# Kernel optimization log

Measured on AMD Instinct MI355X. Metric: run time of the kernel, lower is better.

The kernel has to match this reference:

```python
import jax, jax.numpy as jnp
import numpy as np
import math

D_MODEL = 1024
N_HEADS = 16
HEAD_DIM = D_MODEL // N_HEADS
SEQ_LEN = 8192
INCLUDE_LOCAL = 2


def get_dilated_positions(seq_len, include_local=2):
    # Faithful numpy port of the torch pattern generator (runs once at setup).
    max_attend = include_local + int(math.ceil(math.log2(seq_len + 1)))
    positions = np.zeros((seq_len, max_attend), dtype=np.int64)
    mask = np.zeros((seq_len, max_attend), dtype=bool)
    for i in range(seq_len):
        ap = [i]
        for j in range(1, include_local + 1):
            if i - j >= 0:
                ap.append(i - j)
        k = 2
        while i - 2 ** k >= 0:
            ap.append(i - 2 ** k)
            k += 1
        positions[i, :len(ap)] = ap
        mask[i, :len(ap)] = True
    return positions, mask


def setup_inputs() -> dict:
    key = jax.random.key(0)
    kx, kq, kk, kv, ko = jax.random.split(key, 5)
    x = jax.random.normal(kx, (1, SEQ_LEN, D_MODEL), dtype=jnp.float32)
    # nn.Linear(bias=False) weights, torch layout [out_features, in_features]
    s = 0.02
    q_w = jax.random.normal(kq, (D_MODEL, D_MODEL), dtype=jnp.float32) * s
    k_w = jax.random.normal(kk, (D_MODEL, D_MODEL), dtype=jnp.float32) * s
    v_w = jax.random.normal(kv, (D_MODEL, D_MODEL), dtype=jnp.float32) * s
    o_w = jax.random.normal(ko, (D_MODEL, D_MODEL), dtype=jnp.float32) * s
    pos_np, mask_np = get_dilated_positions(SEQ_LEN, INCLUDE_LOCAL)
    return {
        "x": x,
        "q_w": q_w, "k_w": k_w, "v_w": v_w, "o_w": o_w,
        "positions": jnp.asarray(pos_np),   # (S, A) int64 indices
        "attend_mask": jnp.asarray(mask_np) # (S, A) bool
    }


def reference(x, q_w, k_w, v_w, o_w, positions, attend_mask):
    B, S, _ = x.shape
    H, Dh = N_HEADS, HEAD_DIM
    scale = Dh ** -0.5

    q = (x @ q_w.T).reshape(B, S, H, Dh).transpose(0, 2, 1, 3)  # (B,H,S,Dh)
    k = (x @ k_w.T).reshape(B, S, H, Dh).transpose(0, 2, 1, 3)
    v = (x @ v_w.T).reshape(B, S, H, Dh).transpose(0, 2, 1, 3)

    # Gather K/V at the dilated positions: (B,H,S,A,Dh)
    k_sparse = k[:, :, positions, :]
    v_sparse = v[:, :, positions, :]

    scores = jnp.einsum('bhsd,bhsad->bhsa', q, k_sparse) * scale
    scores = jnp.where(attend_mask[None, None, :, :], scores, -jnp.inf)
    attn = jax.nn.softmax(scores, axis=-1)  # dropout p in eval / 0.0 -> identity

    out = jnp.einsum('bhsa,bhsad->bhsd', attn, v_sparse)
    out = out.transpose(0, 2, 1, 3).reshape(B, S, D_MODEL)
    return out @ o_w.T
```

## Files before the change

### kernel.cpp

```cpp
#include <hip/hip_runtime.h>
#include <hip/hip_bf16.h>

typedef __bf16 bf16_t;
typedef __bf16 bf16x4 __attribute__((ext_vector_type(4)));
typedef __bf16 bf16x8 __attribute__((ext_vector_type(8)));
typedef float floatx16 __attribute__((ext_vector_type(16)));

#define SEQ    8192
#define DM     1024
#define NHEADS 16
#define HDIM   64

__device__ __forceinline__ void async_ld16(bf16_t* lds, const bf16_t* g) {
  __builtin_amdgcn_global_load_lds(
      (__attribute__((address_space(1))) void*)g,
      (__attribute__((address_space(3))) void*)lds, 16, 0, 0);
}

__global__ __launch_bounds__(256)
void cvt_all(const float* __restrict__ x,  const float* __restrict__ qw,
             const float* __restrict__ kw, const float* __restrict__ vw,
             const float* __restrict__ ow,
             bf16_t* __restrict__ Xb,  bf16_t* __restrict__ QWb,
             bf16_t* __restrict__ KWb, bf16_t* __restrict__ VWb,
             bf16_t* __restrict__ OWb) {
  const int b = blockIdx.x;
  const float* in; bf16_t* out; int g;
  if (b < 8192) { in = x; out = Xb; g = b; }
  else {
    const int w  = (b - 8192) >> 10;
    const int wb = (b - 8192) & 1023;
    switch (w) {
      case 0:  in = qw; out = QWb; break;
      case 1:  in = kw; out = KWb; break;
      case 2:  in = vw; out = VWb; break;
      default: in = ow; out = OWb; break;
    }
    g = wb;
  }
  const int idx = (g * 256 + threadIdx.x) * 4;
  float4 v = *(const float4*)(in + idx);
  bf16x4 o = { (bf16_t)v.x, (bf16_t)v.y, (bf16_t)v.z, (bf16_t)v.w };
  *(bf16x4*)(out + idx) = o;
}

template <typename OutT>
__device__ __forceinline__ void gemm_core_256x128(
    const bf16_t* __restrict__ A, const bf16_t* __restrict__ B,
    OutT* __restrict__ C, float scl)
{
  constexpr int Kdim = DM;
  constexpr int NT   = Kdim / 64;
  __shared__ __attribute__((aligned(16))) bf16_t sA[2][256 * 64];
  __shared__ __attribute__((aligned(16))) bf16_t sB[2][128 * 64];

  const int tid  = threadIdx.x;
  const int wave = tid >> 6;
  const int lane = tid & 63;
  const int l31  = lane & 31;
  const int half = lane >> 5;
  const int wm   = wave >> 1;
  const int wn   = wave & 1;

  const int gc = (lane & 7) ^ ((lane >> 3) & 7);
  const size_t arow = (size_t)blockIdx.x * 256 + wave * 8 + (lane >> 3);
  const size_t brow = (size_t)blockIdx.y * 128 + wave * 8 + (lane >> 3);
  const bf16_t* Ag = A + arow * Kdim + gc * 8;
  const bf16_t* Bg = B + brow * Kdim + gc * 8;

  floatx16 acc[2][2];
  #pragma unroll
  for (int i = 0; i < 2; ++i)
    #pragma unroll
    for (int j = 0; j < 2; ++j)
      acc[i][j] = (floatx16)(0.0f);

  #pragma unroll
  for (int j = 0; j < 4; ++j)
    async_ld16(&sA[0][(j * 64 + wave * 8) * 64], Ag + (size_t)j * 64 * Kdim);
  #pragma unroll
  for (int j = 0; j < 2; ++j)
    async_ld16(&sB[0][(j * 64 + wave * 8) * 64], Bg + (size_t)j * 64 * Kdim);
  __syncthreads();

  const int sw = l31 & 7;

  for (int kt = 0; kt < NT; ++kt) {
    const int  cur = kt & 1;
    const int  nxt = cur ^ 1;
    const int  ko  = (kt + 1) * 64;
    const bool pre = (kt + 1 < NT);

    #pragma unroll
    for (int s = 0; s < 4; ++s) {
      const int slot = ((s * 2 + half) ^ sw) * 8;
      bf16x8 af0 = *(const bf16x8*)&sA[cur][(wm * 64      + l31) * 64 + slot];
      bf16x8 af1 = *(const bf16x8*)&sA[cur][(wm * 64 + 32 + l31) * 64 + slot];
      bf16x8 bf0 = *(const bf16x8*)&sB[cur][(wn * 64      + l31) * 64 + slot];
      bf16x8 bf1 = *(const bf16x8*)&sB[cur][(wn * 64 + 32 + l31) * 64 + slot];

      if (pre) {
        if (s == 0) {
          async_ld16(&sA[nxt][(0 * 64 + wave * 8) * 64], Ag + (size_t)0 * 64 * Kdim + ko);
          async_ld16(&sA[nxt][(1 * 64 + wave * 8) * 64], Ag + (size_t)1 * 64 * Kdim + ko);
        } else if (s == 1) {
          async_ld16(&sA[nxt][(2 * 64 + wave * 8) * 64], Ag + (size_t)2 * 64 * Kdim + ko);
          async_ld16(&sA[nxt][(3 * 64 + wave * 8) * 64], Ag + (size_t)3 * 64 * Kdim + ko);
        } else if (s == 2) {
          async_ld16(&sB[nxt][(0 * 64 + wave * 8) * 64], Bg + ko);
          async_ld16(&sB[nxt][(1 * 64 + wave * 8) * 64], Bg + (size_t)64 * Kdim + ko);
        }
      }

      __builtin_amdgcn_s_barrier();
      __builtin_amdgcn_s_setprio(1);
      acc[0][0] = __builtin_amdgcn_mfma_f32_32x32x16_bf16(af0, bf0, acc[0][0], 0, 0, 0);
      acc[0][1] = __builtin_amdgcn_mfma_f32_32x32x16_bf16(af0, bf1, acc[0][1], 0, 0, 0);
      acc[1][0] = __builtin_amdgcn_mfma_f32_32x32x16_bf16(af1, bf0, acc[1][0], 0, 0, 0);
      acc[1][1] = __builtin_amdgcn_mfma_f32_32x32x16_bf16(af1, bf1, acc[1][1], 0, 0, 0);
      __builtin_amdgcn_s_setprio(0);
      if (s < 3) __builtin_amdgcn_s_barrier();
    }

    __syncthreads();
  }

  const int crow0 = blockIdx.x * 256 + wm * 64 + 4 * half;
  const int ccol0 = blockIdx.y * 128 + wn * 64 + l31;
  #pragma unroll
  for (int mi = 0; mi < 2; ++mi)
    #pragma unroll
    for (int ni = 0; ni < 2; ++ni)
      #pragma unroll
      for (int r = 0; r < 16; ++r) {
        const int row = crow0 + mi * 32 + (r & 3) + 8 * (r >> 2);
        C[(size_t)row * DM + (ccol0 + ni * 32)] = (OutT)(acc[mi][ni][r] * scl);
      }
}

__global__ __launch_bounds__(512, 2)
void gemm_qkv(const bf16_t* __restrict__ A,
              const bf16_t* __restrict__ Bq, const bf16_t* __restrict__ Bk,
              const bf16_t* __restrict__ Bv,
              bf16_t* __restrict__ Cq, bf16_t* __restrict__ Ck, bf16_t* __restrict__ Cv)
{
  const bf16_t* B = (blockIdx.z == 0) ? Bq : (blockIdx.z == 1) ? Bk : Bv;
  bf16_t*       C = (blockIdx.z == 0) ? Cq : (blockIdx.z == 1) ? Ck : Cv;
  const float scl = (blockIdx.z == 0) ? 0.125f : 1.0f;
  gemm_core_256x128<bf16_t>(A, B, C, scl);
}

__global__ __launch_bounds__(512, 2)
void gemm_out(const bf16_t* __restrict__ A, const bf16_t* __restrict__ B,
              float* __restrict__ C)
{
  gemm_core_256x128<float>(A, B, C, 1.0f);
}

__global__ __launch_bounds__(256)
void dilated_attn(const bf16_t* __restrict__ Q, const bf16_t* __restrict__ K,
                  const bf16_t* __restrict__ V, bf16_t* O)
{
  __shared__ float sM[2][64];
  __shared__ float sL[2][64];
  __shared__ float sAcc[2][64][17];

  const int lane = threadIdx.x & 63;
  const int wv   = threadIdx.x >> 6;
  const int ql   = wv >> 1;
  const int sub  = wv & 1;
  const int qb   = (blockIdx.x & 7) * 512 + (blockIdx.x >> 3);
  const int i    = qb * 2 + ql;
  const size_t base = (size_t)i * DM + lane * 16;

  bf16x8 q0 = *(const bf16x8*)(Q + base);
  bf16x8 q1 = *(const bf16x8*)(Q + base + 8);
  float qf[16];
  #pragma unroll
  for (int j = 0; j < 8; ++j) { qf[j] = (float)q0[j]; qf[j + 8] = (float)q1[j]; }

  const int npos = (i == 0) ? 1 : (33 - __builtin_clz((unsigned)i));
  auto pos_addr = [&](int t) -> size_t {
    const int off = (t == 0) ? 0 : (1 << (t - 1));
    return (size_t)(i - off) * DM + lane * 16;
  };

  float m = -INFINITY, l = 0.0f;
  float acc[16];
  #pragma unroll
  for (int j = 0; j < 16; ++j) acc[j] = 0.0f;

  int t = sub;
  if (t < npos) {
    size_t a = pos_addr(t);
    bf16x8 k0 = *(const bf16x8*)(K + a), k1 = *(const bf16x8*)(K + a + 8);
    bf16x8 v0 = *(const bf16x8*)(V + a), v1 = *(const bf16x8*)(V + a + 8);
    while (true) {
      const int tn = t + 2;
      const bool more = (tn < npos);
      bf16x8 nk0, nk1, nv0, nv1;
      if (more) {
        const size_t na = pos_addr(tn);
        nk0 = *(const bf16x8*)(K + na); nk1 = *(const bf16x8*)(K + na + 8);
        nv0 = *(const bf16x8*)(V + na); nv1 = *(const bf16x8*)(V + na + 8);
      }

      float sc = 0.0f;
      #pragma unroll
      for (int j = 0; j < 8; ++j) sc += qf[j] * (float)k0[j] + qf[j + 8] * (float)k1[j];
      sc += __shfl_xor(sc, 1, 64);
      sc += __shfl_xor(sc, 2, 64);

      float mn = fmaxf(m, sc);
      float co = __expf(m - mn);
      float w  = __expf(sc - mn);
      l = l * co + w;
      m = mn;
      #pragma unroll
      for (int j = 0; j < 8; ++j) {
        acc[j]     = acc[j]     * co + w * (float)v0[j];
        acc[j + 8] = acc[j + 8] * co + w * (float)v1[j];
      }

      if (!more) break;
      k0 = nk0; k1 = nk1; v0 = nv0; v1 = nv1;
      t = tn;
    }
  }

  if (sub == 1) {
    sM[ql][lane] = m;
    sL[ql][lane] = l;
    #pragma unroll
    for (int j = 0; j < 16; ++j) sAcc[ql][lane][j] = acc[j];
  }
  __syncthreads();
  if (sub == 0) {
    const float mb = sM[ql][lane], lb = sL[ql][lane];
    const float mt = fmaxf(m, mb);
    const float ca = __expf(m - mt);
    const float cb = __expf(mb - mt);
    const float inv = 1.0f / (l * ca + lb * cb);
    bf16x8 o0, o1;
    #pragma unroll
    for (int j = 0; j < 8; ++j) {
      o0[j] = (bf16_t)((acc[j]     * ca + sAcc[ql][lane][j]     * cb) * inv);
      o1[j] = (bf16_t)((acc[j + 8] * ca + sAcc[ql][lane][j + 8] * cb) * inv);
    }
    *(bf16x8*)(O + base)     = o0;
    *(bf16x8*)(O + base + 8) = o1;
  }
}

extern "C" void kernel_launch(void* const* d_in, const int* in_sizes, int n_in,
                              void* d_out, int out_size, void* d_ws, size_t ws_size,
                              hipStream_t stream) {
  (void)in_sizes; (void)n_in; (void)out_size; (void)ws_size;
  const float* x  = (const float*)d_in[0];
  const float* qw = (const float*)d_in[1];
  const float* kw = (const float*)d_in[2];
  const float* vw = (const float*)d_in[3];
  const float* ow = (const float*)d_in[4];
  float* out = (float*)d_out;

  bf16_t* Xb  = (bf16_t*)d_ws;
  bf16_t* Qb  = Xb  + (size_t)SEQ * DM;
  bf16_t* Kb  = Qb  + (size_t)SEQ * DM;
  bf16_t* Vb  = Kb  + (size_t)SEQ * DM;
  bf16_t* QWb = Vb  + (size_t)SEQ * DM;
  bf16_t* KWb = QWb + (size_t)DM * DM;
  bf16_t* VWb = KWb + (size_t)DM * DM;
  bf16_t* OWb = VWb + (size_t)DM * DM;
  bf16_t* AO  = Qb;

  cvt_all<<<dim3(8192 + 4096), dim3(256), 0, stream>>>(x, qw, kw, vw, ow,
                                                       Xb, QWb, KWb, VWb, OWb);

  gemm_qkv<<<dim3(SEQ / 256, DM / 128, 3), dim3(512), 0, stream>>>(Xb, QWb, KWb, VWb, Qb, Kb, Vb);
  dilated_attn<<<dim3(SEQ / 2), dim3(256), 0, stream>>>(Qb, Kb, Vb, AO);
  gemm_out<<<dim3(SEQ / 256, DM / 128), dim3(512), 0, stream>>>(AO, OWb, out);
}
```

Measured before the change: 224.2 us.

## Switch GEMMs to 256x256 tiles with triple-buffered K=32 pipeline

```diff
diff --git a/kernel.cpp b/kernel.cpp
--- a/kernel.cpp
+++ b/kernel.cpp
@@ -45,116 +45,122 @@
 }
 
 template <typename OutT>
-__device__ __forceinline__ void gemm_core_256x128(
-    const bf16_t* __restrict__ A, const bf16_t* __restrict__ B,
-    OutT* __restrict__ C, float scl)
-{
-  constexpr int Kdim = DM;
-  constexpr int NT   = Kdim / 64;
-  __shared__ __attribute__((aligned(16))) bf16_t sA[2][256 * 64];
-  __shared__ __attribute__((aligned(16))) bf16_t sB[2][128 * 64];
+__device__ __forceinline__ void gemm_core_256x256(
+    const bf16_t* __restrict__ A,
+    const bf16_t* __restrict__ B,
+    OutT* __restrict__ C,
+    float scl)
+{
+  constexpr int Kd = DM;
+  constexpr int NT = Kd / 32;
+  __shared__ __attribute__((aligned(16))) bf16_t sA[3][256 * 32];
+  __shared__ __attribute__((aligned(16))) bf16_t sB[3][256 * 32];
 
   const int tid  = threadIdx.x;
   const int wave = tid >> 6;
   const int lane = tid & 63;
   const int l31  = lane & 31;
   const int half = lane >> 5;
-  const int wm   = wave >> 1;
-  const int wn   = wave & 1;
-
-  const int gc = (lane & 7) ^ ((lane >> 3) & 7);
-  const size_t arow = (size_t)blockIdx.x * 256 + wave * 8 + (lane >> 3);
-  const size_t brow = (size_t)blockIdx.y * 128 + wave * 8 + (lane >> 3);
-  const bf16_t* Ag = A + arow * Kdim + gc * 8;
-  const bf16_t* Bg = B + brow * Kdim + gc * 8;
-
-  floatx16 acc[2][2];
-  #pragma unroll
-  for (int i = 0; i < 2; ++i)
+  const int wm   = wave >> 2;
+  const int wn   = wave & 3;
+
+  const int srow = lane >> 2;
+  const int gc   = (lane & 3) ^ (srow & 3);
+  const bf16_t* Ag = A + ((size_t)blockIdx.x * 256 + wave * 32 + srow) * Kd + gc * 8;
+  const bf16_t* Bg = B + ((size_t)wave * 32 + srow) * Kd + gc * 8;
+
+  floatx16 acc[4][2];
+  #pragma unroll
+  for (int i = 0; i < 4; ++i)
     #pragma unroll
     for (int j = 0; j < 2; ++j)
       acc[i][j] = (floatx16)(0.0f);
 
-  #pragma unroll
-  for (int j = 0; j < 4; ++j)
-    async_ld16(&sA[0][(j * 64 + wave * 8) * 64], Ag + (size_t)j * 64 * Kdim);
-  #pragma unroll
-  for (int j = 0; j < 2; ++j)
-    async_ld16(&sB[0][(j * 64 + wave * 8) * 64], Bg + (size_t)j * 64 * Kdim);
-  __syncthreads();
-
-  const int sw = l31 & 7;
-
+  auto stageA = [&](int b, int kt2) {
+    const size_t ko = (size_t)kt2 * 32;
+    async_ld16(&sA[b][(wave * 32)      * 32], Ag + ko);
+    async_ld16(&sA[b][(wave * 32 + 16) * 32], Ag + (size_t)16 * Kd + ko);
+  };
+  auto stageB = [&](int b, int kt2) {
+    const size_t ko = (size_t)kt2 * 32;
+    async_ld16(&sB[b][(wave * 32)      * 32], Bg + ko);
+    async_ld16(&sB[b][(wave * 32 + 16) * 32], Bg + (size_t)16 * Kd + ko);
+  };
+
+  auto phase = [&](int cur, int ks) {
+    const int slot = ((ks * 2 + half) ^ (l31 & 3)) * 8;
+    bf16x8 af[4], bfr[2];
+    #pragma unroll
+    for (int mb = 0; mb < 4; ++mb)
+      af[mb] = *(const bf16x8*)&sA[cur][(wm * 128 + mb * 32 + l31) * 32 + slot];
+    #pragma unroll
+    for (int nb = 0; nb < 2; ++nb)
+      bfr[nb] = *(const bf16x8*)&sB[cur][(wn * 64 + nb * 32 + l31) * 32 + slot];
+    __builtin_amdgcn_s_barrier();
+    __builtin_amdgcn_s_setprio(1);
+    #pragma unroll
+    for (int mb = 0; mb < 4; ++mb)
+      #pragma unroll
+      for (int nb = 0; nb < 2; ++nb)
+        acc[mb][nb] = __builtin_amdgcn_mfma_f32_32x32x16_bf16(af[mb], bfr[nb], acc[mb][nb], 0, 0, 0);
+    __builtin_amdgcn_s_setprio(0);
+  };
+
+  stageA(0, 0); stageB(0, 0);
+  stageA(1, 1); stageB(1, 1);
+  asm volatile("s_waitcnt vmcnt(4)" ::: "memory");
+  __builtin_amdgcn_s_barrier();
+
+  int cur = 0;
   for (int kt = 0; kt < NT; ++kt) {
-    const int  cur = kt & 1;
-    const int  nxt = cur ^ 1;
-    const int  ko  = (kt + 1) * 64;
-    const bool pre = (kt + 1 < NT);
-
-    #pragma unroll
-    for (int s = 0; s < 4; ++s) {
-      const int slot = ((s * 2 + half) ^ sw) * 8;
-      bf16x8 af0 = *(const bf16x8*)&sA[cur][(wm * 64      + l31) * 64 + slot];
-      bf16x8 af1 = *(const bf16x8*)&sA[cur][(wm * 64 + 32 + l31) * 64 + slot];
-      bf16x8 bf0 = *(const bf16x8*)&sB[cur][(wn * 64      + l31) * 64 + slot];
-      bf16x8 bf1 = *(const bf16x8*)&sB[cur][(wn * 64 + 32 + l31) * 64 + slot];
-
-      if (pre) {
-        if (s == 0) {
-          async_ld16(&sA[nxt][(0 * 64 + wave * 8) * 64], Ag + (size_t)0 * 64 * Kdim + ko);
-          async_ld16(&sA[nxt][(1 * 64 + wave * 8) * 64], Ag + (size_t)1 * 64 * Kdim + ko);
-        } else if (s == 1) {
-          async_ld16(&sA[nxt][(2 * 64 + wave * 8) * 64], Ag + (size_t)2 * 64 * Kdim + ko);
-          async_ld16(&sA[nxt][(3 * 64 + wave * 8) * 64], Ag + (size_t)3 * 64 * Kdim + ko);
-        } else if (s == 2) {
-          async_ld16(&sB[nxt][(0 * 64 + wave * 8) * 64], Bg + ko);
-          async_ld16(&sB[nxt][(1 * 64 + wave * 8) * 64], Bg + (size_t)64 * Kdim + ko);
-        }
+    const int  nb2 = (cur >= 1) ? cur - 1 : 2;
+    const bool pre = (kt + 2 < NT);
+
+    if (pre) stageA(nb2, kt + 2);
+    phase(cur, 0);
+    if (pre) stageB(nb2, kt + 2);
+    phase(cur, 1);
+
+    if (kt < NT - 1) {
+      if (kt < NT - 2) asm volatile("s_waitcnt vmcnt(4)" ::: "memory");
+      else             asm volatile("s_waitcnt vmcnt(0)" ::: "memory");
+      __builtin_amdgcn_s_barrier();
+    }
+    cur = (cur == 2) ? 0 : cur + 1;
+  }
+
+  const int crow0 = (int)blockIdx.x * 256 + wm * 128 + 4 * half;
+  const int ccol0 = wn * 64 + l31;
+  #pragma unroll
+  for (int mb = 0; mb < 4; ++mb)
+    #pragma unroll
+    for (int nb = 0; nb < 2; ++nb)
+      #pragma unroll
+      for (int r = 0; r < 16; ++r) {
+        const int row = crow0 + mb * 32 + (r & 3) + 8 * (r >> 2);
+        C[(size_t)row * DM + ccol0 + nb * 32] = (OutT)(acc[mb][nb][r] * scl);
       }
-
-      __builtin_amdgcn_s_barrier();
-      __builtin_amdgcn_s_setprio(1);
-      acc[0][0] = __builtin_amdgcn_mfma_f32_32x32x16_bf16(af0, bf0, acc[0][0], 0, 0, 0);
-      acc[0][1] = __builtin_amdgcn_mfma_f32_32x32x16_bf16(af0, bf1, acc[0][1], 0, 0, 0);
-      acc[1][0] = __builtin_amdgcn_mfma_f32_32x32x16_bf16(af1, bf0, acc[1][0], 0, 0, 0);
-      acc[1][1] = __builtin_amdgcn_mfma_f32_32x32x16_bf16(af1, bf1, acc[1][1], 0, 0, 0);
-      __builtin_amdgcn_s_setprio(0);
-      if (s < 3) __builtin_amdgcn_s_barrier();
-    }
-
-    __syncthreads();
-  }
-
-  const int crow0 = blockIdx.x * 256 + wm * 64 + 4 * half;
-  const int ccol0 = blockIdx.y * 128 + wn * 64 + l31;
-  #pragma unroll
-  for (int mi = 0; mi < 2; ++mi)
-    #pragma unroll
-    for (int ni = 0; ni < 2; ++ni)
-      #pragma unroll
-      for (int r = 0; r < 16; ++r) {
-        const int row = crow0 + mi * 32 + (r & 3) + 8 * (r >> 2);
-        C[(size_t)row * DM + (ccol0 + ni * 32)] = (OutT)(acc[mi][ni][r] * scl);
-      }
 }
 
 __global__ __launch_bounds__(512, 2)
-void gemm_qkv(const bf16_t* __restrict__ A,
-              const bf16_t* __restrict__ Bq, const bf16_t* __restrict__ Bk,
-              const bf16_t* __restrict__ Bv,
-              bf16_t* __restrict__ Cq, bf16_t* __restrict__ Ck, bf16_t* __restrict__ Cv)
-{
-  const bf16_t* B = (blockIdx.z == 0) ? Bq : (blockIdx.z == 1) ? Bk : Bv;
-  bf16_t*       C = (blockIdx.z == 0) ? Cq : (blockIdx.z == 1) ? Ck : Cv;
-  const float scl = (blockIdx.z == 0) ? 0.125f : 1.0f;
-  gemm_core_256x128<bf16_t>(A, B, C, scl);
+void gemm_qkv(const bf16_t* __restrict__ A, const bf16_t* __restrict__ W,
+              bf16_t* __restrict__ Cq)
+{
+  const int y   = blockIdx.y;
+  const int mat = y >> 2;
+  const bf16_t* B = W + (size_t)y * 256 * DM;
+  bf16_t*       C = Cq + (size_t)mat * SEQ * DM + (y & 3) * 256;
+  const float scl = (mat == 0) ? 0.125f : 1.0f;
+  gemm_core_256x256<bf16_t>(A, B, C, scl);
 }
 
 __global__ __launch_bounds__(512, 2)
 void gemm_out(const bf16_t* __restrict__ A, const bf16_t* __restrict__ B,
               float* __restrict__ C)
 {
-  gemm_core_256x128<float>(A, B, C, 1.0f);
+  const bf16_t* Bp = B + (size_t)blockIdx.y * 256 * DM;
+  float*        Cp = C + blockIdx.y * 256;
+  gemm_core_256x256<float>(A, Bp, Cp, 1.0f);
 }
 
 __global__ __launch_bounds__(256)
@@ -276,7 +282,7 @@
   cvt_all<<<dim3(8192 + 4096), dim3(256), 0, stream>>>(x, qw, kw, vw, ow,
                                                        Xb, QWb, KWb, VWb, OWb);
 
-  gemm_qkv<<<dim3(SEQ / 256, DM / 128, 3), dim3(512), 0, stream>>>(Xb, QWb, KWb, VWb, Qb, Kb, Vb);
+  gemm_qkv<<<dim3(SEQ / 256, 12), dim3(512), 0, stream>>>(Xb, QWb, Qb);
   dilated_attn<<<dim3(SEQ / 2), dim3(256), 0, stream>>>(Qb, Kb, Vb, AO);
-  gemm_out<<<dim3(SEQ / 256, DM / 128), dim3(512), 0, stream>>>(AO, OWb, out);
-}
+  gemm_out<<<dim3(SEQ / 256, DM / 256), dim3(512), 0, stream>>>(AO, OWb, out);
+}
```

Result: slower. 287.8 us (+28.4%).

## Restructure GEMM core to 4-wave blocks with templated M tile, single-buffered LDS

Applied to the files above, without the earlier changes.

```diff
diff --git a/kernel.cpp b/kernel.cpp
--- a/kernel.cpp
+++ b/kernel.cpp
@@ -44,15 +44,15 @@
   *(bf16x4*)(out + idx) = o;
 }
 
-template <typename OutT>
-__device__ __forceinline__ void gemm_core_256x128(
+template <int BM, typename OutT>
+__device__ __forceinline__ void gemm_core(
     const bf16_t* __restrict__ A, const bf16_t* __restrict__ B,
     OutT* __restrict__ C, float scl)
 {
-  constexpr int Kdim = DM;
-  constexpr int NT   = Kdim / 64;
-  __shared__ __attribute__((aligned(16))) bf16_t sA[2][256 * 64];
-  __shared__ __attribute__((aligned(16))) bf16_t sB[2][128 * 64];
+  constexpr int Kd  = DM;
+  constexpr int MBF = BM / 64;
+  __shared__ __attribute__((aligned(16))) bf16_t sA[BM * 64];
+  __shared__ __attribute__((aligned(16))) bf16_t sB[128 * 64];
 
   const int tid  = threadIdx.x;
   const int wave = tid >> 6;
@@ -63,82 +63,65 @@
   const int wn   = wave & 1;
 
   const int gc = (lane & 7) ^ ((lane >> 3) & 7);
-  const size_t arow = (size_t)blockIdx.x * 256 + wave * 8 + (lane >> 3);
-  const size_t brow = (size_t)blockIdx.y * 128 + wave * 8 + (lane >> 3);
-  const bf16_t* Ag = A + arow * Kdim + gc * 8;
-  const bf16_t* Bg = B + brow * Kdim + gc * 8;
-
-  floatx16 acc[2][2];
-  #pragma unroll
-  for (int i = 0; i < 2; ++i)
+  const bf16_t* Ag = A + ((size_t)blockIdx.x * BM + wave * 32 + (lane >> 3)) * Kd + gc * 8;
+  const bf16_t* Bg = B + ((size_t)blockIdx.y * 128 + wave * 32 + (lane >> 3)) * Kd + gc * 8;
+
+  floatx16 acc[MBF][2];
+  #pragma unroll
+  for (int i = 0; i < MBF; ++i)
     #pragma unroll
     for (int j = 0; j < 2; ++j)
       acc[i][j] = (floatx16)(0.0f);
 
-  #pragma unroll
-  for (int j = 0; j < 4; ++j)
-    async_ld16(&sA[0][(j * 64 + wave * 8) * 64], Ag + (size_t)j * 64 * Kdim);
-  #pragma unroll
-  for (int j = 0; j < 2; ++j)
-    async_ld16(&sB[0][(j * 64 + wave * 8) * 64], Bg + (size_t)j * 64 * Kdim);
-  __syncthreads();
-
   const int sw = l31 & 7;
 
-  for (int kt = 0; kt < NT; ++kt) {
-    const int  cur = kt & 1;
-    const int  nxt = cur ^ 1;
-    const int  ko  = (kt + 1) * 64;
-    const bool pre = (kt + 1 < NT);
+  for (int ko = 0; ko < Kd; ko += 64) {
+    #pragma unroll
+    for (int h = 0; h < BM / 128; ++h)
+      #pragma unroll
+      for (int n = 0; n < 4; ++n)
+        async_ld16(&sA[(h * 128 + wave * 32 + n * 8) * 64],
+                   Ag + ((size_t)(h * 128 + n * 8)) * Kd + ko);
+    #pragma unroll
+    for (int n = 0; n < 4; ++n)
+      async_ld16(&sB[(wave * 32 + n * 8) * 64], Bg + (size_t)(n * 8) * Kd + ko);
+    __syncthreads();
 
     #pragma unroll
     for (int s = 0; s < 4; ++s) {
       const int slot = ((s * 2 + half) ^ sw) * 8;
-      bf16x8 af0 = *(const bf16x8*)&sA[cur][(wm * 64      + l31) * 64 + slot];
-      bf16x8 af1 = *(const bf16x8*)&sA[cur][(wm * 64 + 32 + l31) * 64 + slot];
-      bf16x8 bf0 = *(const bf16x8*)&sB[cur][(wn * 64      + l31) * 64 + slot];
-      bf16x8 bf1 = *(const bf16x8*)&sB[cur][(wn * 64 + 32 + l31) * 64 + slot];
-
-      if (pre) {
-        if (s == 0) {
-          async_ld16(&sA[nxt][(0 * 64 + wave * 8) * 64], Ag + (size_t)0 * 64 * Kdim + ko);
-          async_ld16(&sA[nxt][(1 * 64 + wave * 8) * 64], Ag + (size_t)1 * 64 * Kdim + ko);
-        } else if (s == 1) {
-          async_ld16(&sA[nxt][(2 * 64 + wave * 8) * 64], Ag + (size_t)2 * 64 * Kdim + ko);
-          async_ld16(&sA[nxt][(3 * 64 + wave * 8) * 64], Ag + (size_t)3 * 64 * Kdim + ko);
-        } else if (s == 2) {
-          async_ld16(&sB[nxt][(0 * 64 + wave * 8) * 64], Bg + ko);
-          async_ld16(&sB[nxt][(1 * 64 + wave * 8) * 64], Bg + (size_t)64 * Kdim + ko);
-        }
+      bf16x8 af[MBF], bfr[2];
+      #pragma unroll
+      for (int mb = 0; mb < MBF; ++mb)
+        af[mb] = *(const bf16x8*)&sA[(wm * (BM / 2) + mb * 32 + l31) * 64 + slot];
+      #pragma unroll
+      for (int nb = 0; nb < 2; ++nb)
+        bfr[nb] = *(const bf16x8*)&sB[(wn * 64 + nb * 32 + l31) * 64 + slot];
+
+      #pragma unroll
+      for (int mb = 0; mb < MBF; ++mb)
+        #pragma unroll
+        for (int nb = 0; nb < 2; ++nb)
+          acc[mb][nb] = __builtin_amdgcn_mfma_f32_32x32x16_bf16(af[mb], bfr[nb], acc[mb][nb], 0, 0, 0);
+    }
+
+    __syncthreads();
+  }
+
+  const int crow0 = (int)blockIdx.x * BM + wm * (BM / 2) + 4 * half;
+  const int ccol0 = (int)blockIdx.y * 128 + wn * 64 + l31;
+  #pragma unroll
+  for (int mb = 0; mb < MBF; ++mb)
+    #pragma unroll
+    for (int nb = 0; nb < 2; ++nb)
+      #pragma unroll
+      for (int r = 0; r < 16; ++r) {
+        const int row = crow0 + mb * 32 + (r & 3) + 8 * (r >> 2);
+        C[(size_t)row * DM + ccol0 + nb * 32] = (OutT)(acc[mb][nb][r] * scl);
       }
-
-      __builtin_amdgcn_s_barrier();
-      __builtin_amdgcn_s_setprio(1);
-      acc[0][0] = __builtin_amdgcn_mfma_f32_32x32x16_bf16(af0, bf0, acc[0][0], 0, 0, 0);
-      acc[0][1] = __builtin_amdgcn_mfma_f32_32x32x16_bf16(af0, bf1, acc[0][1], 0, 0, 0);
-      acc[1][0] = __builtin_amdgcn_mfma_f32_32x32x16_bf16(af1, bf0, acc[1][0], 0, 0, 0);
-      acc[1][1] = __builtin_amdgcn_mfma_f32_32x32x16_bf16(af1, bf1, acc[1][1], 0, 0, 0);
-      __builtin_amdgcn_s_setprio(0);
-      if (s < 3) __builtin_amdgcn_s_barrier();
-    }
-
-    __syncthreads();
-  }
-
-  const int crow0 = blockIdx.x * 256 + wm * 64 + 4 * half;
-  const int ccol0 = blockIdx.y * 128 + wn * 64 + l31;
-  #pragma unroll
-  for (int mi = 0; mi < 2; ++mi)
-    #pragma unroll
-    for (int ni = 0; ni < 2; ++ni)
-      #pragma unroll
-      for (int r = 0; r < 16; ++r) {
-        const int row = crow0 + mi * 32 + (r & 3) + 8 * (r >> 2);
-        C[(size_t)row * DM + (ccol0 + ni * 32)] = (OutT)(acc[mi][ni][r] * scl);
-      }
-}
-
-__global__ __launch_bounds__(512, 2)
+}
+
+__global__ __launch_bounds__(256)
 void gemm_qkv(const bf16_t* __restrict__ A,
               const bf16_t* __restrict__ Bq, const bf16_t* __restrict__ Bk,
               const bf16_t* __restrict__ Bv,
@@ -147,14 +130,14 @@
   const bf16_t* B = (blockIdx.z == 0) ? Bq : (blockIdx.z == 1) ? Bk : Bv;
   bf16_t*       C = (blockIdx.z == 0) ? Cq : (blockIdx.z == 1) ? Ck : Cv;
   const float scl = (blockIdx.z == 0) ? 0.125f : 1.0f;
-  gemm_core_256x128<bf16_t>(A, B, C, scl);
-}
-
-__global__ __launch_bounds__(512, 2)
+  gemm_core<256, bf16_t>(A, B, C, scl);
+}
+
+__global__ __launch_bounds__(256)
 void gemm_out(const bf16_t* __restrict__ A, const bf16_t* __restrict__ B,
               float* __restrict__ C)
 {
-  gemm_core_256x128<float>(A, B, C, 1.0f);
+  gemm_core<128, float>(A, B, C, 1.0f);
 }
 
 __global__ __launch_bounds__(256)
@@ -276,7 +259,7 @@
   cvt_all<<<dim3(8192 + 4096), dim3(256), 0, stream>>>(x, qw, kw, vw, ow,
                                                        Xb, QWb, KWb, VWb, OWb);
 
-  gemm_qkv<<<dim3(SEQ / 256, DM / 128, 3), dim3(512), 0, stream>>>(Xb, QWb, KWb, VWb, Qb, Kb, Vb);
+  gemm_qkv<<<dim3(SEQ / 256, DM / 128, 3), dim3(256), 0, stream>>>(Xb, QWb, KWb, VWb, Qb, Kb, Vb);
   dilated_attn<<<dim3(SEQ / 2), dim3(256), 0, stream>>>(Qb, Kb, Vb, AO);
-  gemm_out<<<dim3(SEQ / 256, DM / 128), dim3(512), 0, stream>>>(AO, OWb, out);
-}
+  gemm_out<<<dim3(SEQ / 128, DM / 128), dim3(256), 0, stream>>>(AO, OWb, out);
+}
```

Result: slower. 237.2 us (+5.8%).
